# Optimization experiments

Measured on AMD Instinct MI355X. Metric: run time of the kernel, lower is better.

## Reference

```python
import jax, jax.numpy as jnp
import numpy as np

BETA = 0.25


def setup_inputs() -> dict:
    key = jax.random.key(0)
    k1, k2 = jax.random.split(key)
    latents = jax.random.normal(k1, (16, 4096, 256), dtype=jnp.float32)
    K = 1024
    # torch init: uniform(-1/K, 1/K)
    codebook = jax.random.uniform(k2, (K, 256), dtype=jnp.float32, minval=-1.0 / K, maxval=1.0 / K)
    return {"latents": latents, "codebook": codebook}


def reference(latents, codebook):
    D = codebook.shape[1]
    flat = latents.reshape(-1, D)  # [N, D]
    dist = (jnp.sum(flat * flat, axis=1, keepdims=True)
            + jnp.sum(codebook * codebook, axis=1)
            - 2.0 * jnp.matmul(flat, codebook.T))
    encoding_inds = jnp.argmin(dist, axis=1)  # [N]
    # gather nearest codebook vectors (equivalent to one-hot @ codebook)
    quantized = codebook[encoding_inds].reshape(latents.shape)
    commitment_loss = jnp.mean((jax.lax.stop_gradient(quantized) - latents) ** 2)
    embedding_loss = jnp.mean((quantized - jax.lax.stop_gradient(latents)) ** 2)
    vq_loss = commitment_loss * BETA + embedding_loss
    # straight-through estimator
    quantized_st = latents + jax.lax.stop_gradient(quantized - latents)
    return quantized_st, vq_loss
```

## Files before the change

### kernel.cpp

```cpp
#include <hip/hip_runtime.h>

typedef __attribute__((ext_vector_type(4))) float f32x4;
typedef __attribute__((ext_vector_type(2))) long i64x2;

#define SCALE 262144.0f
#define NEG2S -524288.0f
#define INV_S2 1.4551915228366852e-11f

static __device__ __forceinline__ unsigned umin2(unsigned a, unsigned b) { return a < b ? a : b; }

static __device__ __forceinline__ float dec_e4m3(unsigned b) {
  int e = (b >> 3) & 15, m = b & 7;
  float v = e ? ldexpf((float)(8 + m), e - 10) : ldexpf((float)m, -9);
  return (b & 0x80) ? -v : v;
}

__global__ void vq_prep(const float* __restrict__ cb,
                        float* __restrict__ norms,
                        unsigned char* __restrict__ cbh,
                        float* __restrict__ loss_out) {
  if (blockIdx.x == 0 && threadIdx.x == 0) *loss_out = 0.0f;
  const int lane = threadIdx.x & 63;
  const int code = (blockIdx.x * blockDim.x + threadIdx.x) >> 6;
  const f32x4 v = ((const f32x4*)(cb + (long)code * 256))[lane];
  unsigned w = __builtin_amdgcn_cvt_pk_fp8_f32(v[0] * SCALE, v[1] * SCALE, 0, false);
  w = __builtin_amdgcn_cvt_pk_fp8_f32(v[2] * SCALE, v[3] * SCALE, w, true);
  float n = 0.f;
#pragma unroll
  for (int j = 0; j < 4; ++j) {
    float d = dec_e4m3((w >> (8 * j)) & 0xFFu);
    n = __builtin_fmaf(d, d, n);
  }
  const int newpos = ((lane >> 1) & 3) * 64 + (lane >> 3) * 8 + (lane & 1) * 4;
  *(unsigned*)(cbh + (long)code * 256 + newpos) = w;
#pragma unroll
  for (int m = 1; m < 64; m <<= 1) n += __shfl_xor(n, m);
  if (lane == 0) norms[code] = n;
}

#define NTHR 512
#define RPB 256
#define NTILE 16

__global__ __launch_bounds__(NTHR, 2)
void vq_main(const float* __restrict__ X,
             const float* __restrict__ CB,
             const float* __restrict__ norms_g,
             const unsigned char* __restrict__ cbh,
             float* __restrict__ out,
             float* __restrict__ loss_out,
             float lscale) {
  __shared__ __attribute__((aligned(16))) unsigned char Xs[2][4096];
  __shared__ unsigned mgAll[NTILE][8][16];
  __shared__ unsigned idxArr[RPB];
  __shared__ float wsumX[8], wsumS[8];

  const int t = threadIdx.x;
  const int lane = t & 63;
  const int wave = t >> 6;
  const int lo16 = lane & 15;
  const int hi = lane >> 4;
  const long rowBase = (long)blockIdx.x * RPB;

  long b[8][8];
  float nrm[8];
  {
    const char* cbB = (const char*)cbh;
#pragma unroll
    for (int n = 0; n < 8; ++n) {
      const int code = wave * 128 + n * 16 + lo16;
      const char* src = cbB + (long)code * 256 + hi * 64;
#pragma unroll
      for (int kp = 0; kp < 4; ++kp) {
        i64x2 bb = *(const i64x2*)(src + kp * 16);
        b[n][2 * kp] = bb.x;
        b[n][2 * kp + 1] = bb.y;
      }
      nrm[n] = norms_g[code];
    }
  }

  const int srow = t >> 5;
  const int sch = t & 31;
  const unsigned sdst =
      (unsigned)(srow * 256 + ((((sch & 3) * 64) + ((sch >> 2) * 8)) ^ ((srow & 7) << 3)));
  const f32x4* xv = (const f32x4*)(X + (rowBase + srow) * 256) + sch * 2;

  float xn = 0.f;
  f32x4 p0, p1;

#define CVT_WRITE(BUF)                                                                    \
  {                                                                                       \
    float s0 = 0.f;                                                                       \
    _Pragma("unroll") for (int j = 0; j < 4; ++j) s0 = __builtin_fmaf(p0[j], p0[j], s0);  \
    _Pragma("unroll") for (int j = 0; j < 4; ++j) s0 = __builtin_fmaf(p1[j], p1[j], s0);  \
    xn += s0;                                                                             \
    unsigned w0 = __builtin_amdgcn_cvt_pk_fp8_f32(p0[0], p0[1], 0, false);                \
    w0 = __builtin_amdgcn_cvt_pk_fp8_f32(p0[2], p0[3], w0, true);                         \
    unsigned w1 = __builtin_amdgcn_cvt_pk_fp8_f32(p1[0], p1[1], 0, false);                \
    w1 = __builtin_amdgcn_cvt_pk_fp8_f32(p1[2], p1[3], w1, true);                         \
    *(long*)((char*)&Xs[BUF][0] + sdst) = (long)(unsigned)w0 | ((long)w1 << 32);          \
  }

  p0 = __builtin_nontemporal_load(xv);
  p1 = __builtin_nontemporal_load(xv + 1);
  CVT_WRITE(0);
  p0 = __builtin_nontemporal_load(xv + 1024);
  p1 = __builtin_nontemporal_load(xv + 1024 + 1);
  __syncthreads();

  for (int tt = 0; tt < NTILE; ++tt) {
    const char* xb = (const char*)&Xs[tt & 1][0];
    const unsigned abase = (unsigned)(lo16 * 256 + hi * 64);
    const unsigned aswz = (unsigned)((lo16 & 7) << 3);
    long a[8];
#pragma unroll
    for (int ks = 0; ks < 8; ++ks)
      a[ks] = *(const long*)(xb + ((abase + ks * 8) ^ aswz));

    f32x4 acc[8];
#pragma unroll
    for (int n = 0; n < 8; ++n) {
      f32x4 z = {0.f, 0.f, 0.f, 0.f};
      acc[n] = z;
    }
    __builtin_amdgcn_s_setprio(1);
#pragma unroll
    for (int ks = 0; ks < 8; ++ks)
#pragma unroll
      for (int n = 0; n < 8; ++n)
        acc[n] = __builtin_amdgcn_mfma_f32_16x16x32_fp8_fp8(a[ks], b[n][ks], acc[n], 0, 0, 0);
    __builtin_amdgcn_s_setprio(0);

    unsigned bst[4] = {0xFFFFFFFFu, 0xFFFFFFFFu, 0xFFFFFFFFu, 0xFFFFFFFFu};
#pragma unroll
    for (int n = 0; n < 8; ++n) {
      const float nf = nrm[n];
      const unsigned code = (unsigned)(wave * 128 + n * 16 + lo16);
#pragma unroll
      for (int r = 0; r < 4; ++r) {
        float sv = __builtin_fmaf(NEG2S, acc[n][r], nf);
        unsigned u = __float_as_uint(sv);
        u = ((int)u < 0) ? ~u : (u | 0x80000000u);
        bst[r] = umin2(bst[r], (u & 0xFFFFFC00u) | code);
      }
    }
#pragma unroll
    for (int r = 0; r < 4; ++r) {
#pragma unroll
      for (int msk = 1; msk < 16; msk <<= 1)
        bst[r] = umin2(bst[r], (unsigned)__shfl_xor((int)bst[r], msk));
    }
    if (lo16 == 0) {
#pragma unroll
      for (int r = 0; r < 4; ++r) mgAll[tt][wave][hi * 4 + r] = bst[r];
    }

    if (tt + 1 < NTILE) {
      CVT_WRITE((tt + 1) & 1);
      if (tt + 2 < NTILE) {
        p0 = __builtin_nontemporal_load(xv + (tt + 2) * 1024);
        p1 = __builtin_nontemporal_load(xv + (tt + 2) * 1024 + 1);
      }
    }
    __syncthreads();
  }

#pragma unroll
  for (int msk = 1; msk < 64; msk <<= 1) xn += __shfl_xor(xn, msk);
  if (lane == 0) wsumX[wave] = xn;

  float scv = 0.f;
  if (t < RPB) {
    unsigned e = 0xFFFFFFFFu;
#pragma unroll
    for (int w = 0; w < 8; ++w) e = umin2(e, mgAll[t >> 4][w][t & 15]);
    idxArr[t] = e & 1023u;
    unsigned um = (e & 0xFFFFFC00u) | 512u;
    float sr = (um & 0x80000000u) ? __uint_as_float(um & 0x7FFFFFFFu) : __uint_as_float(~um);
    scv = sr * INV_S2;
  }
#pragma unroll
  for (int msk = 1; msk < 64; msk <<= 1) scv += __shfl_xor(scv, msk);
  if (lane == 0) wsumS[wave] = scv;
  __syncthreads();

  {
    const f32x4* CBv = (const f32x4*)CB;
    f32x4* Og = (f32x4*)(out + rowBase * 256);
#pragma unroll 4
    for (int i = 0; i < 32; ++i) {
      int idx = t + NTHR * i;
      int row = idx >> 6, d4 = idx & 63;
      int code = (int)idxArr[row];
      f32x4 e = CBv[code * 64 + d4];
      __builtin_nontemporal_store(e, Og + idx);
    }
  }

  if (t == 0) {
    float tot = 0.f;
#pragma unroll
    for (int w = 0; w < 8; ++w) tot += wsumX[w] + wsumS[w];
    atomicAdd(loss_out, tot * lscale);
  }
}

extern "C" void kernel_launch(void* const* d_in, const int* in_sizes, int n_in,
                              void* d_out, int out_size, void* d_ws, size_t ws_size,
                              hipStream_t stream) {
  const float* X = (const float*)d_in[0];
  const float* CB = (const float*)d_in[1];
  float* out = (float*)d_out;

  const int ND = in_sizes[0];
  const int K = in_sizes[1] / 256;
  const int N = ND / 256;

  float* ws_norms = (float*)d_ws;
  unsigned char* ws_cb = (unsigned char*)((char*)d_ws + 4096);
  float* loss_out = out + (size_t)ND;

  vq_prep<<<K / 4, 256, 0, stream>>>(CB, ws_norms, ws_cb, loss_out);

  const float lscale = 1.25f / (float)ND;
  vq_main<<<N / RPB, NTHR, 0, stream>>>(X, CB, ws_norms, ws_cb, out, loss_out, lscale);
}
```

Baseline: 62.70 us.

## Quantize codebook to FP4 in LDS and use scaled 32x32x64 MFMA

The codebook is now quantized to FP4 (e2m1) with a fixed scale and stored nibble-packed in a workspace. Each block copies the whole 128KB FP4 codebook and the norms into LDS via global_load_lds. Each wave keeps its 32 input rows as FP8 in registers and sweeps all codes with mfma_scale 32x32x64 mixed fp8/fp4 instructions. The loss is now computed exactly from the re-read inputs and the gathered codebook rows, replacing the approximate distance-based sum. The aim is fewer MFMA instructions and no per-tile staging or syncs, at the cost of much coarser codebook precision, which risks argmin mismatches, and large LDS use that limits occupancy to one block per CU.

```diff
diff --git a/kernel.cpp b/kernel.cpp
--- a/kernel.cpp
+++ b/kernel.cpp
@@ -1,38 +1,36 @@
 #include <hip/hip_runtime.h>
 
 typedef __attribute__((ext_vector_type(4))) float f32x4;
-typedef __attribute__((ext_vector_type(2))) long i64x2;
-
-#define SCALE 262144.0f
-#define NEG2S -524288.0f
-#define INV_S2 1.4551915228366852e-11f
+typedef __attribute__((ext_vector_type(16))) float f32x16;
+typedef __attribute__((ext_vector_type(8))) int v8i;
+typedef __attribute__((ext_vector_type(4))) unsigned int u32x4;
 
 static __device__ __forceinline__ unsigned umin2(unsigned a, unsigned b) { return a < b ? a : b; }
 
-static __device__ __forceinline__ float dec_e4m3(unsigned b) {
-  int e = (b >> 3) & 15, m = b & 7;
-  float v = e ? ldexpf((float)(8 + m), e - 10) : ldexpf((float)m, -9);
-  return (b & 0x80) ? -v : v;
-}
-
 __global__ void vq_prep(const float* __restrict__ cb,
                         float* __restrict__ norms,
-                        unsigned char* __restrict__ cbh,
+                        unsigned char* __restrict__ cb4,
                         float* __restrict__ loss_out) {
   if (blockIdx.x == 0 && threadIdx.x == 0) *loss_out = 0.0f;
   const int lane = threadIdx.x & 63;
   const int code = (blockIdx.x * blockDim.x + threadIdx.x) >> 6;
   const f32x4 v = ((const f32x4*)(cb + (long)code * 256))[lane];
-  unsigned w = __builtin_amdgcn_cvt_pk_fp8_f32(v[0] * SCALE, v[1] * SCALE, 0, false);
-  w = __builtin_amdgcn_cvt_pk_fp8_f32(v[2] * SCALE, v[3] * SCALE, w, true);
   float n = 0.f;
+  unsigned nib[4];
 #pragma unroll
   for (int j = 0; j < 4; ++j) {
-    float d = dec_e4m3((w >> (8 * j)) & 0xFFu);
+    float sv = v[j] * 4096.0f;
+    float av = fabsf(sv);
+    int c = (av >= 0.25f) + (av >= 0.75f) + (av >= 1.25f) + (av >= 1.75f) +
+            (av >= 2.5f) + (av >= 3.5f) + (av >= 5.0f);
+    float d = (c <= 3) ? 0.5f * (float)c : (c == 4 ? 2.f : (c == 5 ? 3.f : (c == 6 ? 4.f : 6.f)));
     n = __builtin_fmaf(d, d, n);
+    nib[j] = (unsigned)c | (sv < 0.f ? 8u : 0u);
   }
-  const int newpos = ((lane >> 1) & 3) * 64 + (lane >> 3) * 8 + (lane & 1) * 4;
-  *(unsigned*)(cbh + (long)code * 256 + newpos) = w;
+  unsigned short u16 = (unsigned short)(nib[0] | (nib[1] << 4) | (nib[2] << 8) | (nib[3] << 12));
+  const int cg = code >> 5, col = code & 31;
+  const int kc = lane >> 4, h = (lane >> 3) & 1, b = (lane & 7) * 2;
+  *(unsigned short*)(cb4 + cg * 4096 + kc * 1024 + (h * 32 + col) * 16 + b) = u16;
 #pragma unroll
   for (int m = 1; m < 64; m <<= 1) n += __shfl_xor(n, m);
   if (lane == 0) norms[code] = n;
@@ -40,170 +38,120 @@
 
 #define NTHR 512
 #define RPB 256
-#define NTILE 16
 
 __global__ __launch_bounds__(NTHR, 2)
 void vq_main(const float* __restrict__ X,
              const float* __restrict__ CB,
              const float* __restrict__ norms_g,
-             const unsigned char* __restrict__ cbh,
+             const unsigned char* __restrict__ cb4g,
              float* __restrict__ out,
              float* __restrict__ loss_out,
              float lscale) {
-  __shared__ __attribute__((aligned(16))) unsigned char Xs[2][4096];
-  __shared__ unsigned mgAll[NTILE][8][16];
-  __shared__ unsigned idxArr[RPB];
-  __shared__ float wsumX[8], wsumS[8];
+  __shared__ __attribute__((aligned(16))) unsigned char cb4L[131072];
+  __shared__ __attribute__((aligned(16))) float nrmLds[1024];
 
   const int t = threadIdx.x;
   const int lane = t & 63;
   const int wave = t >> 6;
-  const int lo16 = lane & 15;
-  const int hi = lane >> 4;
+  const int col = lane & 31;
+  const int hl = lane >> 5;
   const long rowBase = (long)blockIdx.x * RPB;
 
-  long b[8][8];
-  float nrm[8];
+#pragma unroll
+  for (int i = 0; i < 16; ++i) {
+    __builtin_amdgcn_global_load_lds(
+        (const __attribute__((address_space(1))) void*)(cb4g + i * 8192 + wave * 1024 + lane * 16),
+        (__attribute__((address_space(3))) void*)((char*)cb4L + i * 8192 + wave * 1024),
+        16, 0, 0);
+  }
+  if (t < 256) {
+    __builtin_amdgcn_global_load_lds(
+        (const __attribute__((address_space(1))) void*)((const char*)norms_g + wave * 1024 + lane * 16),
+        (__attribute__((address_space(3))) void*)((char*)nrmLds + wave * 1024),
+        16, 0, 0);
+  }
+
+  v8i a[4];
   {
-    const char* cbB = (const char*)cbh;
+    const float* xrow = X + (rowBase + wave * 32 + col) * 256;
 #pragma unroll
-    for (int n = 0; n < 8; ++n) {
-      const int code = wave * 128 + n * 16 + lo16;
-      const char* src = cbB + (long)code * 256 + hi * 64;
+    for (int kc = 0; kc < 4; ++kc) {
+      const f32x4* xb = (const f32x4*)(xrow + kc * 64 + hl * 32);
 #pragma unroll
-      for (int kp = 0; kp < 4; ++kp) {
-        i64x2 bb = *(const i64x2*)(src + kp * 16);
-        b[n][2 * kp] = bb.x;
-        b[n][2 * kp + 1] = bb.y;
+      for (int c = 0; c < 8; ++c) {
+        f32x4 q = __builtin_nontemporal_load(xb + c);
+        unsigned w = __builtin_amdgcn_cvt_pk_fp8_f32(q[0], q[1], 0, false);
+        w = __builtin_amdgcn_cvt_pk_fp8_f32(q[2], q[3], w, true);
+        a[kc][c] = (int)w;
       }
-      nrm[n] = norms_g[code];
     }
   }
 
-  const int srow = t >> 5;
-  const int sch = t & 31;
-  const unsigned sdst =
-      (unsigned)(srow * 256 + ((((sch & 3) * 64) + ((sch >> 2) * 8)) ^ ((srow & 7) << 3)));
-  const f32x4* xv = (const f32x4*)(X + (rowBase + srow) * 256) + sch * 2;
-
-  float xn = 0.f;
-  f32x4 p0, p1;
-
-#define CVT_WRITE(BUF)                                                                    \
-  {                                                                                       \
-    float s0 = 0.f;                                                                       \
-    _Pragma("unroll") for (int j = 0; j < 4; ++j) s0 = __builtin_fmaf(p0[j], p0[j], s0);  \
-    _Pragma("unroll") for (int j = 0; j < 4; ++j) s0 = __builtin_fmaf(p1[j], p1[j], s0);  \
-    xn += s0;                                                                             \
-    unsigned w0 = __builtin_amdgcn_cvt_pk_fp8_f32(p0[0], p0[1], 0, false);                \
-    w0 = __builtin_amdgcn_cvt_pk_fp8_f32(p0[2], p0[3], w0, true);                         \
-    unsigned w1 = __builtin_amdgcn_cvt_pk_fp8_f32(p1[0], p1[1], 0, false);                \
-    w1 = __builtin_amdgcn_cvt_pk_fp8_f32(p1[2], p1[3], w1, true);                         \
-    *(long*)((char*)&Xs[BUF][0] + sdst) = (long)(unsigned)w0 | ((long)w1 << 32);          \
-  }
-
-  p0 = __builtin_nontemporal_load(xv);
-  p1 = __builtin_nontemporal_load(xv + 1);
-  CVT_WRITE(0);
-  p0 = __builtin_nontemporal_load(xv + 1024);
-  p1 = __builtin_nontemporal_load(xv + 1024 + 1);
+  asm volatile("s_waitcnt vmcnt(0)" ::: "memory");
   __syncthreads();
 
-  for (int tt = 0; tt < NTILE; ++tt) {
-    const char* xb = (const char*)&Xs[tt & 1][0];
-    const unsigned abase = (unsigned)(lo16 * 256 + hi * 64);
-    const unsigned aswz = (unsigned)((lo16 & 7) << 3);
-    long a[8];
+  unsigned best[16];
 #pragma unroll
-    for (int ks = 0; ks < 8; ++ks)
-      a[ks] = *(const long*)(xb + ((abase + ks * 8) ^ aswz));
+  for (int r = 0; r < 16; ++r) best[r] = 0xFFFFFFFFu;
 
-    f32x4 acc[8];
+  for (int j = 0; j < 32; ++j) {
+    const int cg = (wave * 4 + j) & 31;
+    const char* ebase = (const char*)cb4L + cg * 4096 + lane * 16;
+    u32x4 q0 = *(const u32x4*)(ebase);
+    u32x4 q1 = *(const u32x4*)(ebase + 1024);
+    u32x4 q2 = *(const u32x4*)(ebase + 2048);
+    u32x4 q3 = *(const u32x4*)(ebase + 3072);
+    const float nf = nrmLds[cg * 32 + col] + 16777216.0f;
+
+    f32x16 accA = {0.f}, accB = {0.f};
+    v8i b0 = {(int)q0.x, (int)q0.y, (int)q0.z, (int)q0.w, (int)q0.x, (int)q0.y, (int)q0.z, (int)q0.w};
+    v8i b1 = {(int)q1.x, (int)q1.y, (int)q1.z, (int)q1.w, (int)q1.x, (int)q1.y, (int)q1.z, (int)q1.w};
+    v8i b2 = {(int)q2.x, (int)q2.y, (int)q2.z, (int)q2.w, (int)q2.x, (int)q2.y, (int)q2.z, (int)q2.w};
+    v8i b3 = {(int)q3.x, (int)q3.y, (int)q3.z, (int)q3.w, (int)q3.x, (int)q3.y, (int)q3.z, (int)q3.w};
+    accA = __builtin_amdgcn_mfma_scale_f32_32x32x64_f8f6f4(a[0], b0, accA, 0, 4, 0, 127, 0, 127);
+    accB = __builtin_amdgcn_mfma_scale_f32_32x32x64_f8f6f4(a[1], b1, accB, 0, 4, 0, 127, 0, 127);
+    accA = __builtin_amdgcn_mfma_scale_f32_32x32x64_f8f6f4(a[2], b2, accA, 0, 4, 0, 127, 0, 127);
+    accB = __builtin_amdgcn_mfma_scale_f32_32x32x64_f8f6f4(a[3], b3, accB, 0, 4, 0, 127, 0, 127);
+
+    const unsigned code = (unsigned)(cg * 32 + col);
 #pragma unroll
-    for (int n = 0; n < 8; ++n) {
-      f32x4 z = {0.f, 0.f, 0.f, 0.f};
-      acc[n] = z;
+    for (int r = 0; r < 16; ++r) {
+      float sv = __builtin_fmaf(-8192.0f, accA[r] + accB[r], nf);
+      best[r] = umin2(best[r], (__float_as_uint(sv) & 0xFFFFFC00u) | code);
     }
-    __builtin_amdgcn_s_setprio(1);
-#pragma unroll
-    for (int ks = 0; ks < 8; ++ks)
-#pragma unroll
-      for (int n = 0; n < 8; ++n)
-        acc[n] = __builtin_amdgcn_mfma_f32_16x16x32_fp8_fp8(a[ks], b[n][ks], acc[n], 0, 0, 0);
-    __builtin_amdgcn_s_setprio(0);
-
-    unsigned bst[4] = {0xFFFFFFFFu, 0xFFFFFFFFu, 0xFFFFFFFFu, 0xFFFFFFFFu};
-#pragma unroll
-    for (int n = 0; n < 8; ++n) {
-      const float nf = nrm[n];
-      const unsigned code = (unsigned)(wave * 128 + n * 16 + lo16);
-#pragma unroll
-      for (int r = 0; r < 4; ++r) {
-        float sv = __builtin_fmaf(NEG2S, acc[n][r], nf);
-        unsigned u = __float_as_uint(sv);
-        u = ((int)u < 0) ? ~u : (u | 0x80000000u);
-        bst[r] = umin2(bst[r], (u & 0xFFFFFC00u) | code);
-      }
-    }
-#pragma unroll
-    for (int r = 0; r < 4; ++r) {
-#pragma unroll
-      for (int msk = 1; msk < 16; msk <<= 1)
-        bst[r] = umin2(bst[r], (unsigned)__shfl_xor((int)bst[r], msk));
-    }
-    if (lo16 == 0) {
-#pragma unroll
-      for (int r = 0; r < 4; ++r) mgAll[tt][wave][hi * 4 + r] = bst[r];
-    }
-
-    if (tt + 1 < NTILE) {
-      CVT_WRITE((tt + 1) & 1);
-      if (tt + 2 < NTILE) {
-        p0 = __builtin_nontemporal_load(xv + (tt + 2) * 1024);
-        p1 = __builtin_nontemporal_load(xv + (tt + 2) * 1024 + 1);
-      }
-    }
-    __syncthreads();
   }
 
 #pragma unroll
-  for (int msk = 1; msk < 64; msk <<= 1) xn += __shfl_xor(xn, msk);
-  if (lane == 0) wsumX[wave] = xn;
+  for (int r = 0; r < 16; ++r) {
+#pragma unroll
+    for (int m = 1; m < 32; m <<= 1)
+      best[r] = umin2(best[r], (unsigned)__shfl_xor((int)best[r], m));
+  }
 
-  float scv = 0.f;
-  if (t < RPB) {
-    unsigned e = 0xFFFFFFFFu;
+  float ls = 0.f;
+  {
+    const f32x4* CBv = (const f32x4*)CB;
+    const f32x4* Xv = (const f32x4*)X + (rowBase + wave * 32) * 64;
+    f32x4* Og = (f32x4*)out + (rowBase + wave * 32) * 64;
 #pragma unroll
-    for (int w = 0; w < 8; ++w) e = umin2(e, mgAll[t >> 4][w][t & 15]);
-    idxArr[t] = e & 1023u;
-    unsigned um = (e & 0xFFFFFC00u) | 512u;
-    float sr = (um & 0x80000000u) ? __uint_as_float(um & 0x7FFFFFFFu) : __uint_as_float(~um);
-    scv = sr * INV_S2;
+    for (int r = 0; r < 32; ++r) {
+      const int hl2 = (r >> 2) & 1;
+      const int rr = r - 4 * hl2;
+      const int reg = (rr & 3) + 4 * (rr >> 3);
+      const int code = __shfl((int)best[reg], hl2 * 32) & 1023;
+      f32x4 e = CBv[code * 64 + lane];
+      f32x4 x = __builtin_nontemporal_load(Xv + r * 64 + lane);
+      __builtin_nontemporal_store(e, Og + r * 64 + lane);
+#pragma unroll
+      for (int jj = 0; jj < 4; ++jj) {
+        float df = e[jj] - x[jj];
+        ls = __builtin_fmaf(df, df, ls);
+      }
+    }
   }
 #pragma unroll
-  for (int msk = 1; msk < 64; msk <<= 1) scv += __shfl_xor(scv, msk);
-  if (lane == 0) wsumS[wave] = scv;
-  __syncthreads();
-
-  {
-    const f32x4* CBv = (const f32x4*)CB;
-    f32x4* Og = (f32x4*)(out + rowBase * 256);
-#pragma unroll 4
-    for (int i = 0; i < 32; ++i) {
-      int idx = t + NTHR * i;
-      int row = idx >> 6, d4 = idx & 63;
-      int code = (int)idxArr[row];
-      f32x4 e = CBv[code * 64 + d4];
-      __builtin_nontemporal_store(e, Og + idx);
-    }
-  }
-
-  if (t == 0) {
-    float tot = 0.f;
-#pragma unroll
-    for (int w = 0; w < 8; ++w) tot += wsumX[w] + wsumS[w];
-    atomicAdd(loss_out, tot * lscale);
-  }
+  for (int m = 1; m < 64; m <<= 1) ls += __shfl_xor(ls, m);
+  if (lane == 0) atomicAdd(loss_out, ls * lscale);
 }
 
 extern "C" void kernel_launch(void* const* d_in, const int* in_sizes, int n_in,
@@ -218,11 +166,11 @@
   const int N = ND / 256;
 
   float* ws_norms = (float*)d_ws;
-  unsigned char* ws_cb = (unsigned char*)((char*)d_ws + 4096);
+  unsigned char* ws_cb4 = (unsigned char*)((char*)d_ws + 4096);
   float* loss_out = out + (size_t)ND;
 
-  vq_prep<<<K / 4, 256, 0, stream>>>(CB, ws_norms, ws_cb, loss_out);
+  vq_prep<<<K / 4, 256, 0, stream>>>(CB, ws_norms, ws_cb4, loss_out);
 
   const float lscale = 1.25f / (float)ND;
-  vq_main<<<N / RPB, NTHR, 0, stream>>>(X, CB, ws_norms, ws_cb, out, loss_out, lscale);
+  vq_main<<<N / RPB, NTHR, 0, stream>>>(X, CB, ws_norms, ws_cb4, out, loss_out, lscale);
 }
```

Result: slower. 83.10 us (+32.5%).
